# Performance work log

Measured on AMD Instinct MI355X. Metric: run time of the kernel, lower is better.

## Reference

```python
import jax, jax.numpy as jnp
import numpy as np


def _conv1x1(x, w, b):
    # x: [B, Cin, H, W], w: [Cout, Cin], b: [Cout]
    return jnp.einsum('oi,bihw->bohw', w, x) + b[None, :, None, None]


def setup_inputs() -> dict:
    key = jax.random.key(0)
    ks = jax.random.split(key, 16)
    B, H, W = 32, 512, 512
    img = jax.random.normal(ks[0], (B, 3, H, W), dtype=jnp.float32)
    mask = jax.random.uniform(ks[1], (B, 1, H, W), dtype=jnp.float32)

    def init_conv(k, cout, cin):
        k1, k2 = jax.random.split(k)
        bound = 1.0 / np.sqrt(cin)  # PyTorch Conv2d default init range
        w = jax.random.uniform(k1, (cout, cin), minval=-bound, maxval=bound, dtype=jnp.float32)
        b = jax.random.uniform(k2, (cout,), minval=-bound, maxval=bound, dtype=jnp.float32)
        return w, b

    qi_w, qi_b = init_conv(ks[2], 1, 3)
    ki_w, ki_b = init_conv(ks[3], 1, 3)
    vi_w, vi_b = init_conv(ks[4], 3, 3)
    qr_w, qr_b = init_conv(ks[5], 1, 1)
    kr_w, kr_b = init_conv(ks[6], 1, 1)
    vr_w, vr_b = init_conv(ks[7], 1, 1)
    fu_w, fu_b = init_conv(ks[8], 3, 6)
    return {
        'img': img, 'mask': mask,
        'qi_w': qi_w, 'qi_b': qi_b, 'ki_w': ki_w, 'ki_b': ki_b,
        'vi_w': vi_w, 'vi_b': vi_b, 'qr_w': qr_w, 'qr_b': qr_b,
        'kr_w': kr_w, 'kr_b': kr_b, 'vr_w': vr_w, 'vr_b': vr_b,
        'fu_w': fu_w, 'fu_b': fu_b,
    }


def reference(img, mask, qi_w, qi_b, ki_w, ki_b, vi_w, vi_b,
              qr_w, qr_b, kr_w, kr_b, vr_w, vr_b, fu_w, fu_b):
    q_i = _conv1x1(img, qi_w, qi_b)    # [B,1,H,W]
    k_i = _conv1x1(img, ki_w, ki_b)    # [B,1,H,W]
    v_i = _conv1x1(img, vi_w, vi_b)    # [B,3,H,W]
    q_r = _conv1x1(mask, qr_w, qr_b)   # [B,1,H,W]
    k_r = _conv1x1(mask, kr_w, kr_b)   # [B,1,H,W]
    v_r = _conv1x1(mask, vr_w, vr_b)   # [B,1,H,W]
    # broadcasting: the v_r terms are 1-channel and broadcast to 3 channels
    f_i = jax.nn.sigmoid(q_i * k_i) * v_i + jax.nn.sigmoid(q_i * k_r) * v_r  # [B,3,H,W]
    f_r = jax.nn.sigmoid(q_r * k_r) * v_r + jax.nn.sigmoid(q_r * k_i) * v_i  # [B,3,H,W]
    f_f = _conv1x1(jnp.concatenate([f_i, f_r], axis=1), fu_w, fu_b)          # [B,3,H,W]
    return f_f
```

## Files before the change

### kernel.cpp

```cpp
#include <hip/hip_runtime.h>
#include <math.h>


#define HW_SHIFT  18
#define HWQ_SHIFT 16
#define HWQ (1 << HWQ_SHIFT)

__device__ __forceinline__ float sigm(float x) {
    return __builtin_amdgcn_rcpf(1.0f + __expf(-x));
}

__global__ __launch_bounds__(256) void rim_kernel(
    const float* __restrict__ img,  const float* __restrict__ mask,
    const float* __restrict__ qiw,  const float* __restrict__ qib,
    const float* __restrict__ kiw,  const float* __restrict__ kib,
    const float* __restrict__ viw,  const float* __restrict__ vib,
    const float* __restrict__ qrw,  const float* __restrict__ qrb,
    const float* __restrict__ krw,  const float* __restrict__ krb,
    const float* __restrict__ vrw,  const float* __restrict__ vrb,
    const float* __restrict__ fuw,  const float* __restrict__ fub,
    float* __restrict__ out)
{
    const float w_qi0 = qiw[0], w_qi1 = qiw[1], w_qi2 = qiw[2], b_qi = qib[0];
    const float w_ki0 = kiw[0], w_ki1 = kiw[1], w_ki2 = kiw[2], b_ki = kib[0];
    float w_vi[9], b_vi[3];
#pragma unroll
    for (int j = 0; j < 9; ++j) w_vi[j] = viw[j];
#pragma unroll
    for (int j = 0; j < 3; ++j) b_vi[j] = vib[j];
    const float w_qr = qrw[0], b_qr = qrb[0];
    const float w_kr = krw[0], b_kr = krb[0];
    const float w_vr = vrw[0], b_vr = vrb[0];
    float w_fu[18], b_fu[3];
#pragma unroll
    for (int j = 0; j < 18; ++j) w_fu[j] = fuw[j];
#pragma unroll
    for (int j = 0; j < 3; ++j) b_fu[j] = fub[j];

    const int g0  = blockIdx.x * 512 + threadIdx.x;
    const int b   = g0 >> HWQ_SHIFT;
    const int hw0 = g0 & (HWQ - 1);
    const int hw1 = hw0 + 256;

    const float4* ip = (const float4*)(img  + ((size_t)b * 3 << HW_SHIFT));
    const float4* mp = (const float4*)(mask + ((size_t)b     << HW_SHIFT));

    float4 xa0 = ip[hw0];
    float4 xa1 = ip[hw0 + HWQ];
    float4 xa2 = ip[hw0 + 2 * HWQ];
    float4 mqa = mp[hw0];
    float4 xb0 = ip[hw1];
    float4 xb1 = ip[hw1 + HWQ];
    float4 xb2 = ip[hw1 + 2 * HWQ];
    float4 mqb = mp[hw1];

    auto compute = [&](const float4& X0q, const float4& X1q, const float4& X2q,
                       const float4& Mq, float4& O0, float4& O1, float4& O2) {
        const float* px0 = &X0q.x; const float* px1 = &X1q.x;
        const float* px2 = &X2q.x; const float* pm  = &Mq.x;
        float* po0 = &O0.x; float* po1 = &O1.x; float* po2 = &O2.x;
#pragma unroll
        for (int l = 0; l < 4; ++l) {
            const float X0 = px0[l], X1 = px1[l], X2 = px2[l], M = pm[l];

            const float q_i = b_qi + w_qi0 * X0 + w_qi1 * X1 + w_qi2 * X2;
            const float k_i = b_ki + w_ki0 * X0 + w_ki1 * X1 + w_ki2 * X2;
            const float v0  = b_vi[0] + w_vi[0] * X0 + w_vi[1] * X1 + w_vi[2] * X2;
            const float v1  = b_vi[1] + w_vi[3] * X0 + w_vi[4] * X1 + w_vi[5] * X2;
            const float v2  = b_vi[2] + w_vi[6] * X0 + w_vi[7] * X1 + w_vi[8] * X2;
            const float q_r = b_qr + w_qr * M;
            const float k_r = b_kr + w_kr * M;
            const float v_r = b_vr + w_vr * M;

            const float s_ii = sigm(q_i * k_i);
            const float s_ir = sigm(q_i * k_r);
            const float s_rr = sigm(q_r * k_r);
            const float s_ri = sigm(q_r * k_i);

            const float fi0 = s_ii * v0 + s_ir * v_r;
            const float fi1 = s_ii * v1 + s_ir * v_r;
            const float fi2 = s_ii * v2 + s_ir * v_r;
            const float fr0 = s_rr * v_r + s_ri * v0;
            const float fr1 = s_rr * v_r + s_ri * v1;
            const float fr2 = s_rr * v_r + s_ri * v2;

            po0[l] = b_fu[0] + w_fu[0]  * fi0 + w_fu[1]  * fi1 + w_fu[2]  * fi2
                             + w_fu[3]  * fr0 + w_fu[4]  * fr1 + w_fu[5]  * fr2;
            po1[l] = b_fu[1] + w_fu[6]  * fi0 + w_fu[7]  * fi1 + w_fu[8]  * fi2
                             + w_fu[9]  * fr0 + w_fu[10] * fr1 + w_fu[11] * fr2;
            po2[l] = b_fu[2] + w_fu[12] * fi0 + w_fu[13] * fi1 + w_fu[14] * fi2
                             + w_fu[15] * fr0 + w_fu[16] * fr1 + w_fu[17] * fr2;
        }
    };

    float4* op = (float4*)(out + ((size_t)b * 3 << HW_SHIFT));

    float4 o0, o1, o2;
    compute(xa0, xa1, xa2, mqa, o0, o1, o2);
    op[hw0]           = o0;
    op[hw0 + HWQ]     = o1;
    op[hw0 + 2 * HWQ] = o2;

    compute(xb0, xb1, xb2, mqb, o0, o1, o2);
    op[hw1]           = o0;
    op[hw1 + HWQ]     = o1;
    op[hw1 + 2 * HWQ] = o2;
}

extern "C" void kernel_launch(void* const* d_in, const int* in_sizes, int n_in,
                              void* d_out, int out_size, void* d_ws, size_t ws_size,
                              hipStream_t stream) {
    const float* img  = (const float*)d_in[0];
    const float* mask = (const float*)d_in[1];
    const float* qiw  = (const float*)d_in[2];
    const float* qib  = (const float*)d_in[3];
    const float* kiw  = (const float*)d_in[4];
    const float* kib  = (const float*)d_in[5];
    const float* viw  = (const float*)d_in[6];
    const float* vib  = (const float*)d_in[7];
    const float* qrw  = (const float*)d_in[8];
    const float* qrb  = (const float*)d_in[9];
    const float* krw  = (const float*)d_in[10];
    const float* krb  = (const float*)d_in[11];
    const float* vrw  = (const float*)d_in[12];
    const float* vrb  = (const float*)d_in[13];
    const float* fuw  = (const float*)d_in[14];
    const float* fub  = (const float*)d_in[15];
    float* out = (float*)d_out;

    rim_kernel<<<4096, 256, 0, stream>>>(img, mask, qiw, qib, kiw, kib, viw, vib,
                                         qrw, qrb, krw, krb, vrw, vrb, fuw, fub, out);
}
```

Measured before the change: 229.4 us.

## Double-buffer global-to-LDS async loads with eight tiles per block

Each block now processes eight 256-float4 tiles instead of two. Inputs are staged through a double-buffered LDS area using direct global_load_lds instructions, with manual vmcnt waits, so the loads for the next tile overlap the compute and stores of the current one. The grid shrinks from 4096 to 1024 blocks. This aims to keep more memory traffic in flight per wave, in exchange for LDS use, hand-counted vmcnt synchronisation that must also account for stores, and fewer blocks in the grid.

```diff
diff --git a/kernel.cpp b/kernel.cpp
--- a/kernel.cpp
+++ b/kernel.cpp
@@ -2,13 +2,19 @@
 #include <math.h>
 
 
-#define HW_SHIFT  18
 #define HWQ_SHIFT 16
 #define HWQ (1 << HWQ_SHIFT)
 
 __device__ __forceinline__ float sigm(float x) {
     return __builtin_amdgcn_rcpf(1.0f + __expf(-x));
 }
+
+#define GLD_LDS16(gp, lp) \
+    __builtin_amdgcn_global_load_lds( \
+        (const __attribute__((address_space(1))) unsigned int*)(gp), \
+        (__attribute__((address_space(3))) unsigned int*)(lp), 16, 0, 0)
+
+#define WAITVM(N) asm volatile("s_waitcnt vmcnt(" #N ")" ::: "memory")
 
 __global__ __launch_bounds__(256) void rim_kernel(
     const float* __restrict__ img,  const float* __restrict__ mask,
@@ -21,6 +27,8 @@
     const float* __restrict__ fuw,  const float* __restrict__ fub,
     float* __restrict__ out)
 {
+    __shared__ float4 lds[2][4][256];
+
     const float w_qi0 = qiw[0], w_qi1 = qiw[1], w_qi2 = qiw[2], b_qi = qib[0];
     const float w_ki0 = kiw[0], w_ki1 = kiw[1], w_ki2 = kiw[2], b_ki = kib[0];
     float w_vi[9], b_vi[3];
@@ -37,22 +45,15 @@
 #pragma unroll
     for (int j = 0; j < 3; ++j) b_fu[j] = fub[j];
 
-    const int g0  = blockIdx.x * 512 + threadIdx.x;
-    const int b   = g0 >> HWQ_SHIFT;
-    const int hw0 = g0 & (HWQ - 1);
-    const int hw1 = hw0 + 256;
+    const int tid  = threadIdx.x;
+    const int wv   = tid & ~63;
+    const int gblk = blockIdx.x * 2048;
+    const int b    = gblk >> HWQ_SHIFT;
+    const int hw   = (gblk & (HWQ - 1)) + tid;
 
-    const float4* ip = (const float4*)(img  + ((size_t)b * 3 << HW_SHIFT));
-    const float4* mp = (const float4*)(mask + ((size_t)b     << HW_SHIFT));
-
-    float4 xa0 = ip[hw0];
-    float4 xa1 = ip[hw0 + HWQ];
-    float4 xa2 = ip[hw0 + 2 * HWQ];
-    float4 mqa = mp[hw0];
-    float4 xb0 = ip[hw1];
-    float4 xb1 = ip[hw1 + HWQ];
-    float4 xb2 = ip[hw1 + 2 * HWQ];
-    float4 mqb = mp[hw1];
+    const float4* ip4 = (const float4*)img  + ((size_t)b * 3 << HWQ_SHIFT);
+    const float4* mp4 = (const float4*)mask + ((size_t)b     << HWQ_SHIFT);
+    float4*       op4 = (float4*)out        + ((size_t)b * 3 << HWQ_SHIFT);
 
     auto compute = [&](const float4& X0q, const float4& X1q, const float4& X2q,
                        const float4& Mq, float4& O0, float4& O1, float4& O2) {
@@ -93,18 +94,38 @@
         }
     };
 
-    float4* op = (float4*)(out + ((size_t)b * 3 << HW_SHIFT));
+#define PREF(d, t) do { \
+        const float4* gp = ip4 + hw + (t) * 256; \
+        GLD_LDS16(gp,            &lds[d][0][wv]); \
+        GLD_LDS16(gp + HWQ,      &lds[d][1][wv]); \
+        GLD_LDS16(gp + 2 * HWQ,  &lds[d][2][wv]); \
+        GLD_LDS16(mp4 + hw + (t) * 256, &lds[d][3][wv]); \
+    } while (0)
 
-    float4 o0, o1, o2;
-    compute(xa0, xa1, xa2, mqa, o0, o1, o2);
-    op[hw0]           = o0;
-    op[hw0 + HWQ]     = o1;
-    op[hw0 + 2 * HWQ] = o2;
+#define COMP(d, t) do { \
+        const float4 X0q = lds[d][0][tid]; \
+        const float4 X1q = lds[d][1][tid]; \
+        const float4 X2q = lds[d][2][tid]; \
+        const float4 Mq  = lds[d][3][tid]; \
+        float4 o0, o1, o2; \
+        compute(X0q, X1q, X2q, Mq, o0, o1, o2); \
+        op4[hw + (t) * 256]           = o0; \
+        op4[hw + (t) * 256 + HWQ]     = o1; \
+        op4[hw + (t) * 256 + 2 * HWQ] = o2; \
+    } while (0)
 
-    compute(xb0, xb1, xb2, mqb, o0, o1, o2);
-    op[hw1]           = o0;
-    op[hw1 + HWQ]     = o1;
-    op[hw1 + 2 * HWQ] = o2;
+    PREF(0, 0);
+    PREF(1, 1); WAITVM(4); COMP(0, 0);
+    PREF(0, 2); WAITVM(7); COMP(1, 1);
+    PREF(1, 3); WAITVM(7); COMP(0, 2);
+    PREF(0, 4); WAITVM(7); COMP(1, 3);
+    PREF(1, 5); WAITVM(7); COMP(0, 4);
+    PREF(0, 6); WAITVM(7); COMP(1, 5);
+    PREF(1, 7); WAITVM(7); COMP(0, 6);
+                WAITVM(3); COMP(1, 7);
+
+#undef PREF
+#undef COMP
 }
 
 extern "C" void kernel_launch(void* const* d_in, const int* in_sizes, int n_in,
@@ -128,6 +149,6 @@
     const float* fub  = (const float*)d_in[15];
     float* out = (float*)d_out;
 
-    rim_kernel<<<4096, 256, 0, stream>>>(img, mask, qiw, qib, kiw, kib, viw, vib,
+    rim_kernel<<<1024, 256, 0, stream>>>(img, mask, qiw, qib, kiw, kib, viw, vib,
                                          qrw, qrb, krw, krb, vrw, vrb, fuw, fub, out);
 }
```

Result: slower. 238.4 us (+3.9%).

## Switch to persistent-style blocks with double-buffered software-pipelined loads

Applied to the files above, without the earlier changes.

Cuts the grid from 4096 blocks of 256 threads to 256 blocks of 512 threads, with each thread handling 16 float4 pixel groups instead of 2. Loads for the next iteration are issued before the current one is computed and stored (ping-pong A/B registers), to hide memory latency and amortize the per-thread weight loads. The risk is that only 256 blocks on a many-CU GPU may underfill the device and lower memory-level parallelism compared to the large grid.

```diff
diff --git a/kernel.cpp b/kernel.cpp
--- a/kernel.cpp
+++ b/kernel.cpp
@@ -2,7 +2,6 @@
 #include <math.h>
 
 
-#define HW_SHIFT  18
 #define HWQ_SHIFT 16
 #define HWQ (1 << HWQ_SHIFT)
 
@@ -10,7 +9,7 @@
     return __builtin_amdgcn_rcpf(1.0f + __expf(-x));
 }
 
-__global__ __launch_bounds__(256) void rim_kernel(
+__global__ __launch_bounds__(512, 2) void rim_kernel(
     const float* __restrict__ img,  const float* __restrict__ mask,
     const float* __restrict__ qiw,  const float* __restrict__ qib,
     const float* __restrict__ kiw,  const float* __restrict__ kib,
@@ -37,31 +36,22 @@
 #pragma unroll
     for (int j = 0; j < 3; ++j) b_fu[j] = fub[j];
 
-    const int g0  = blockIdx.x * 512 + threadIdx.x;
-    const int b   = g0 >> HWQ_SHIFT;
-    const int hw0 = g0 & (HWQ - 1);
-    const int hw1 = hw0 + 256;
+    const int bid   = blockIdx.x;
+    const int b     = bid >> 3;
+    const int base  = (bid & 7) * 8192 + threadIdx.x;
 
-    const float4* ip = (const float4*)(img  + ((size_t)b * 3 << HW_SHIFT));
-    const float4* mp = (const float4*)(mask + ((size_t)b     << HW_SHIFT));
-
-    float4 xa0 = ip[hw0];
-    float4 xa1 = ip[hw0 + HWQ];
-    float4 xa2 = ip[hw0 + 2 * HWQ];
-    float4 mqa = mp[hw0];
-    float4 xb0 = ip[hw1];
-    float4 xb1 = ip[hw1 + HWQ];
-    float4 xb2 = ip[hw1 + 2 * HWQ];
-    float4 mqb = mp[hw1];
+    const float4* px = (const float4*)img  + ((size_t)b * 3 << HWQ_SHIFT) + base;
+    const float4* pm = (const float4*)mask + ((size_t)b     << HWQ_SHIFT) + base;
+    float4*       po = (float4*)out        + ((size_t)b * 3 << HWQ_SHIFT) + base;
 
     auto compute = [&](const float4& X0q, const float4& X1q, const float4& X2q,
                        const float4& Mq, float4& O0, float4& O1, float4& O2) {
         const float* px0 = &X0q.x; const float* px1 = &X1q.x;
-        const float* px2 = &X2q.x; const float* pm  = &Mq.x;
+        const float* px2 = &X2q.x; const float* pmq = &Mq.x;
         float* po0 = &O0.x; float* po1 = &O1.x; float* po2 = &O2.x;
 #pragma unroll
         for (int l = 0; l < 4; ++l) {
-            const float X0 = px0[l], X1 = px1[l], X2 = px2[l], M = pm[l];
+            const float X0 = px0[l], X1 = px1[l], X2 = px2[l], M = pmq[l];
 
             const float q_i = b_qi + w_qi0 * X0 + w_qi1 * X1 + w_qi2 * X2;
             const float k_i = b_ki + w_ki0 * X0 + w_ki1 * X1 + w_ki2 * X2;
@@ -93,18 +83,33 @@
         }
     };
 
-    float4* op = (float4*)(out + ((size_t)b * 3 << HW_SHIFT));
+    float4 Ax0, Ax1, Ax2, Am;
+    float4 Bx0, Bx1, Bx2, Bm;
+    float4 o0, o1, o2;
 
-    float4 o0, o1, o2;
-    compute(xa0, xa1, xa2, mqa, o0, o1, o2);
-    op[hw0]           = o0;
-    op[hw0 + HWQ]     = o1;
-    op[hw0 + 2 * HWQ] = o2;
+#define LOADS(P, t) \
+    P##x0 = px[(t) * 512]; \
+    P##x1 = px[(t) * 512 + HWQ]; \
+    P##x2 = px[(t) * 512 + 2 * HWQ]; \
+    P##m  = pm[(t) * 512];
 
-    compute(xb0, xb1, xb2, mqb, o0, o1, o2);
-    op[hw1]           = o0;
-    op[hw1 + HWQ]     = o1;
-    op[hw1 + 2 * HWQ] = o2;
+#define CSTORE(P, t) \
+    compute(P##x0, P##x1, P##x2, P##m, o0, o1, o2); \
+    po[(t) * 512]           = o0; \
+    po[(t) * 512 + HWQ]     = o1; \
+    po[(t) * 512 + 2 * HWQ] = o2;
+
+    LOADS(A, 0)
+#pragma unroll
+    for (int t = 0; t < 16; t += 2) {
+        LOADS(B, t + 1)
+        CSTORE(A, t)
+        if (t + 2 < 16) { LOADS(A, t + 2) }
+        CSTORE(B, t + 1)
+    }
+
+#undef LOADS
+#undef CSTORE
 }
 
 extern "C" void kernel_launch(void* const* d_in, const int* in_sizes, int n_in,
@@ -128,6 +133,6 @@
     const float* fub  = (const float*)d_in[15];
     float* out = (float*)d_out;
 
-    rim_kernel<<<4096, 256, 0, stream>>>(img, mask, qiw, qib, kiw, kib, viw, vib,
-                                         qrw, qrb, krw, krb, vrw, vrb, fuw, fub, out);
+    rim_kernel<<<256, 512, 0, stream>>>(img, mask, qiw, qib, kiw, kib, viw, vib,
+                                        qrw, qrb, krw, krb, vrw, vrb, fuw, fub, out);
 }
```

New measurement: 239.0 us. 1.04x slower.
